# Kernel tuning notes

Measured on AMD Instinct MI355X. Metric: run time of the kernel, lower is better.

The kernel has to match this reference:

```python
import jax, jax.numpy as jnp
import numpy as np

NUM_HEADS = 16
HEAD_DIM = 128  # 2048 / 16


def setup_inputs() -> dict:
    key = jax.random.key(0)
    ks = jax.random.split(key, 5)
    B, S, D = 2, 2048, 2048
    scale = 1.0 / np.sqrt(D)
    return {
        "x": jax.random.normal(ks[0], (B, S, D), dtype=jnp.float32),
        "Wq": jax.random.normal(ks[1], (D, D), dtype=jnp.float32) * scale,
        "Wk": jax.random.normal(ks[2], (D, D), dtype=jnp.float32) * scale,
        "Wv": jax.random.normal(ks[3], (D, D), dtype=jnp.float32) * scale,
        "Wo": jax.random.normal(ks[4], (D, D), dtype=jnp.float32) * scale,
    }


def reference(x, Wq, Wk, Wv, Wo):
    B, S, D = x.shape
    H, Hd = NUM_HEADS, HEAD_DIM
    # nn.Linear(bias=False): y = x @ W.T
    q = (x @ Wq.T).reshape(B, S, H, Hd).transpose(0, 2, 1, 3)  # [B,H,S,Hd]
    k = (x @ Wk.T).reshape(B, S, H, Hd).transpose(0, 2, 1, 3)
    v = (x @ Wv.T).reshape(B, S, H, Hd).transpose(0, 2, 1, 3)
    scores = jnp.einsum("bhqd,bhkd->bhqk", q, k) / jnp.sqrt(jnp.float32(Hd))
    attn = jax.nn.softmax(scores, axis=-1)  # dropout p=0 (eval) -> identity
    out = jnp.einsum("bhqk,bhkd->bhqd", attn, v)  # [B,H,S,Hd]
    out = out.transpose(0, 2, 1, 3).reshape(B, S, D)
    out = out @ Wo.T
    return out
```

## Files before the change

kernel.cpp:

```cpp
#include <hip/hip_runtime.h>
#include <math.h>
#include <stdint.h>


#define DDIM 2048
#define SEQ  2048
#define NH   16
#define HD   128

typedef __attribute__((ext_vector_type(4))) float f32x4;
typedef __attribute__((ext_vector_type(16))) float f32x16;
typedef __attribute__((ext_vector_type(8))) __bf16 bf16x8;
typedef __attribute__((ext_vector_type(4))) unsigned int u32x4;
typedef __attribute__((ext_vector_type(2))) unsigned int u32x2;

#define MFMA_B16(a, b, c) __builtin_amdgcn_mfma_f32_16x16x32_bf16((a), (b), (c), 0, 0, 0)
#define MFMA32(a, b, c) __builtin_amdgcn_mfma_f32_32x32x16_bf16((a), (b), (c), 0, 0, 0)

__device__ __forceinline__ void async16(const void* g, void* l) {
  __builtin_amdgcn_global_load_lds(
      (const __attribute__((address_space(1))) unsigned int*)g,
      (__attribute__((address_space(3))) unsigned int*)l, 16, 0, 0);
}

__device__ __forceinline__ unsigned short f2bf(float f) {
  unsigned u = __builtin_bit_cast(unsigned, f);
  u += 0x7fffu + ((u >> 16) & 1u);
  return (unsigned short)(u >> 16);
}

__device__ __forceinline__ bf16x8 ldfrag(const unsigned short* p) {
  return __builtin_bit_cast(bf16x8, *(const u32x4*)p);
}

__device__ __forceinline__ void cvt_body(const float* __restrict__ s,
                                         unsigned short* __restrict__ d, int i) {
  const f32x4* sp = (const f32x4*)s;
  f32x4 a = sp[2 * i], b = sp[2 * i + 1];
  u32x4 o;
  o.x = ((unsigned)f2bf(a.y) << 16) | f2bf(a.x);
  o.y = ((unsigned)f2bf(a.w) << 16) | f2bf(a.z);
  o.z = ((unsigned)f2bf(b.y) << 16) | f2bf(b.x);
  o.w = ((unsigned)f2bf(b.w) << 16) | f2bf(b.z);
  ((u32x4*)d)[i] = o;
}

__global__ __launch_bounds__(256) void cvt_bf16_kernel(const float* __restrict__ s,
                                                       unsigned short* __restrict__ d) {
  cvt_body(s, d, blockIdx.x * 256 + threadIdx.x);
}

__global__ __launch_bounds__(256) void cvt_all_kernel(const float* __restrict__ x,
                                                      const float* __restrict__ wq,
                                                      const float* __restrict__ wk,
                                                      const float* __restrict__ wv,
                                                      const float* __restrict__ wo,
                                                      unsigned short* __restrict__ xb,
                                                      unsigned short* __restrict__ wqkv,
                                                      unsigned short* __restrict__ wob) {
  const int b = blockIdx.x;
  if (b < 4096) {
    cvt_body(x, xb, b * 256 + threadIdx.x);
  } else if (b < 10240) {
    const int wi = (b - 4096) >> 11, lb = (b - 4096) & 2047;
    const float* s = (wi == 0) ? wq : (wi == 1) ? wk : wv;
    cvt_body(s, wqkv + (size_t)wi * 4194304u, lb * 256 + threadIdx.x);
  } else {
    cvt_body(wo, wob, (b - 10240) * 256 + threadIdx.x);
  }
}

#define STGA(BUF, KH, COL)                            \
  {                                                   \
    const int c_ = (COL) & 2047;                      \
    async16(pA[0] + c_, &As[BUF][KH][tid * 8]);       \
    async16(pA[1] + c_, &As[BUF][KH][4096 + tid * 8]);\
  }
#define STGB(BUF, KH, COL)                            \
  {                                                   \
    const int c_ = (COL) & 2047;                      \
    async16(pB[0] + c_, &Bs[BUF][KH][tid * 8]);       \
    async16(pB[1] + c_, &Bs[BUF][KH][4096 + tid * 8]);\
  }
#define VM8 asm volatile("s_waitcnt vmcnt(8)" ::: "memory")
#define VMNONE (void)0

#define PHASE(BUF, KH, NH, STAGE_STMT, WAIT_STMT)                 \
  {                                                               \
    if ((NH) == 0) {                                              \
      const unsigned short* pl = &As[BUF][KH][0];                 \
      _Pragma("unroll") for (int mf = 0; mf < 4; ++mf) {          \
        const int r = awbase + mf * 32;                           \
        af[mf][0] = ldfrag(pl + r * 32 + c0);                     \
        af[mf][1] = ldfrag(pl + r * 32 + c1);                     \
      }                                                           \
    }                                                             \
    {                                                             \
      const unsigned short* pl = &Bs[BUF][KH][0];                 \
      const int r = bwbase + (NH) * 32;                           \
      bf0 = ldfrag(pl + r * 32 + c0);                             \
      bf1 = ldfrag(pl + r * 32 + c1);                             \
    }                                                             \
    STAGE_STMT;                                                   \
    __builtin_amdgcn_s_barrier();                                 \
    asm volatile("s_waitcnt lgkmcnt(0)" ::: "memory");            \
    __builtin_amdgcn_sched_barrier(0);                            \
    __builtin_amdgcn_s_setprio(1);                                \
    _Pragma("unroll") for (int mf = 0; mf < 4; ++mf) {            \
      acc[mf][NH] = MFMA32(af[mf][0], bf0, acc[mf][NH]);          \
      acc[mf][NH] = MFMA32(af[mf][1], bf1, acc[mf][NH]);          \
    }                                                             \
    __builtin_amdgcn_s_setprio(0);                                \
    WAIT_STMT;                                                    \
    __builtin_amdgcn_s_barrier();                                 \
  }

__global__ __launch_bounds__(512) void gemm_qkv8(const unsigned short* __restrict__ A,
                                                 const unsigned short* __restrict__ B,
                                                 unsigned short* __restrict__ Oqk,
                                                 unsigned short* __restrict__ Ovt,
                                                 float alpha_q) {
  __shared__ unsigned short As[2][2][256 * 32];
  __shared__ unsigned short Bs[2][2][256 * 32];
  const int tid = threadIdx.x;
  const int lane = tid & 63, w = tid >> 6;
  const int l32 = lane & 31, half = lane >> 5;
  const int wr = w >> 2, wc = w & 3;
  const int bm = blockIdx.y * 256, bn = blockIdx.x * 256;

  const int f2 = (l32 >> 1) & 3;
  const int c0 = (half ^ f2) * 8;
  const int c1 = ((2 + half) ^ f2) * 8;
  const int awbase = wr * 128 + l32;
  const int bwbase = wc * 64 + l32;

  f32x16 acc[4][2];
#pragma unroll
  for (int mf = 0; mf < 4; ++mf)
#pragma unroll
    for (int nf = 0; nf < 2; ++nf)
#pragma unroll
      for (int e = 0; e < 16; ++e) acc[mf][nf][e] = 0.f;

  bf16x8 af[4][2];
  bf16x8 bf0, bf1;

  const unsigned short* pA[2];
  const unsigned short* pB[2];
#pragma unroll
  for (int j = 0; j < 2; ++j) {
    const int slot = j * 512 + tid;
    const int row = slot >> 2, cs = slot & 3;
    const int g = cs ^ ((row >> 1) & 3);
    pA[j] = A + (size_t)(bm + row) * DDIM + g * 8;
    pB[j] = B + (size_t)(bn + row) * DDIM + g * 8;
  }

  STGA(0, 0, 0);
  STGB(0, 0, 0);
  STGA(0, 1, 32);
  STGB(0, 1, 32);
  STGA(1, 0, 64);
  STGB(1, 0, 64);
  asm volatile("s_waitcnt vmcnt(8)" ::: "memory");
  __builtin_amdgcn_s_barrier();

#pragma unroll 1
  for (int j = 0; j < 16; ++j) {
    const int cb = j * 128;
    PHASE(0, 0, 0, STGA(1, 1, cb + 96), VMNONE);
    PHASE(0, 0, 1, STGB(1, 1, cb + 96), VM8);
    PHASE(0, 1, 0, STGA(0, 0, cb + 128), VMNONE);
    PHASE(0, 1, 1, STGB(0, 0, cb + 128), VM8);
    PHASE(1, 0, 0, STGA(0, 1, cb + 160), VMNONE);
    PHASE(1, 0, 1, STGB(0, 1, cb + 160), VM8);
    PHASE(1, 1, 0, STGA(1, 0, cb + 192), VMNONE);
    PHASE(1, 1, 1, STGB(1, 0, cb + 192), VM8);
  }
  asm volatile("s_waitcnt vmcnt(0)" ::: "memory");

  const int seg = bn >> 11;
  const int bnl = bn & 2047;
  const float alpha = (seg == 0) ? alpha_q : 1.0f;
#pragma unroll
  for (int mf = 0; mf < 4; ++mf) {
#pragma unroll
    for (int nf = 0; nf < 2; ++nf) {
#pragma unroll
      for (int rg = 0; rg < 4; ++rg) {
        const int m0 = bm + wr * 128 + mf * 32 + rg * 8 + half * 4;
        const float v0 = acc[mf][nf][rg * 4 + 0] * alpha;
        const float v1 = acc[mf][nf][rg * 4 + 1] * alpha;
        const float v2 = acc[mf][nf][rg * 4 + 2] * alpha;
        const float v3 = acc[mf][nf][rg * 4 + 3] * alpha;
        const int n = bnl + wc * 64 + nf * 32 + l32;
        if (seg < 2) {
          unsigned short* O = Oqk + (size_t)seg * (4096u * 2048u);
          O[(size_t)(m0 + 0) * DDIM + n] = f2bf(v0);
          O[(size_t)(m0 + 1) * DDIM + n] = f2bf(v1);
          O[(size_t)(m0 + 2) * DDIM + n] = f2bf(v2);
          O[(size_t)(m0 + 3) * DDIM + n] = f2bf(v3);
        } else {
          const int bb = m0 >> 11, s0 = m0 & 2047;
          const int hh = n >> 7, dd = n & 127;
          u32x2 st;
          st.x = ((unsigned)f2bf(v1) << 16) | f2bf(v0);
          st.y = ((unsigned)f2bf(v3) << 16) | f2bf(v2);
          *(u32x2*)&Ovt[((size_t)((bb * NH + hh) * HD + dd)) * SEQ + s0] = st;
        }
      }
    }
  }
}

__global__ __launch_bounds__(256) void gemm_o64(const unsigned short* __restrict__ A,
                                                const unsigned short* __restrict__ B,
                                                float* __restrict__ Cf) {
  __shared__ unsigned short As[128 * 64];
  __shared__ unsigned short Bs[64 * 64];
  const int tid = threadIdx.x;
  const int lane = tid & 63, w = tid >> 6;
  const int l32 = lane & 31, half = lane >> 5;
  const int wm = (w >> 1) * 64, wn = (w & 1) * 32;
  const int bm = blockIdx.y * 128, bn = blockIdx.x * 64;

  f32x16 acc[2];
#pragma unroll
  for (int i = 0; i < 2; ++i)
#pragma unroll
    for (int e = 0; e < 16; ++e) acc[i][e] = 0.f;

  const unsigned short* pa[4];
  const unsigned short* pbb[2];
  {
#pragma unroll
    for (int j = 0; j < 4; ++j) {
      const int row = j * 32 + (tid >> 3);
      const int cg = (tid & 7) ^ (row & 7) ^ ((row >> 3) & 7);
      pa[j] = A + (size_t)(bm + row) * DDIM + cg * 8;
      if (j < 2) pbb[j] = B + (size_t)(bn + row) * DDIM + cg * 8;
    }
  }

  const int fr = (l32 & 7) ^ (l32 >> 3);
  const int fb = fr ^ ((wn >> 3) & 4);

  for (int kt = 0; kt < 32; ++kt) {
    __syncthreads();
#pragma unroll
    for (int j = 0; j < 4; ++j) {
      async16(pa[j], &As[(j * 256 + tid) * 8]);
      pa[j] += 64;
      if (j < 2) {
        async16(pbb[j], &Bs[(j * 256 + tid) * 8]);
        pbb[j] += 64;
      }
    }
    __syncthreads();
#pragma unroll
    for (int ks = 0; ks < 4; ++ks) {
      const int ph = ks * 2 + half;
      bf16x8 af0 = ldfrag(&As[(wm + l32) * 64 + (ph ^ fr) * 8]);
      bf16x8 af1 = ldfrag(&As[(wm + 32 + l32) * 64 + (ph ^ fr ^ 4) * 8]);
      bf16x8 bf0 = ldfrag(&Bs[(wn + l32) * 64 + (ph ^ fb) * 8]);
      acc[0] = MFMA32(af0, bf0, acc[0]);
      acc[1] = MFMA32(af1, bf0, acc[1]);
    }
  }

#pragma unroll
  for (int i = 0; i < 2; ++i) {
#pragma unroll
    for (int rg = 0; rg < 4; ++rg) {
      const int m0 = bm + wm + i * 32 + rg * 8 + half * 4;
      const int n = bn + wn + l32;
      Cf[(size_t)(m0 + 0) * DDIM + n] = acc[i][rg * 4 + 0];
      Cf[(size_t)(m0 + 1) * DDIM + n] = acc[i][rg * 4 + 1];
      Cf[(size_t)(m0 + 2) * DDIM + n] = acc[i][rg * 4 + 2];
      Cf[(size_t)(m0 + 3) * DDIM + n] = acc[i][rg * 4 + 3];
    }
  }
}

__global__ __launch_bounds__(512) void attn_kernel(const unsigned short* __restrict__ qb,
                                                   const unsigned short* __restrict__ kb,
                                                   const unsigned short* __restrict__ vtb,
                                                   unsigned short* __restrict__ ab) {
  __shared__ unsigned short Ks[64 * 128];
  __shared__ unsigned short Vts[128 * 64];
  __shared__ unsigned short Pw[8 * 16 * 40];
  const int tid = threadIdx.x;
  const int w = tid >> 6, lane = tid & 63;
  const int quad = lane >> 4, l16 = lane & 15;
  const int qt = blockIdx.x, bh = blockIdx.y;
  const int b = bh >> 4, h = bh & 15;
  const int qrow = qt * 128 + w * 16 + l16;

  const unsigned short* qp = qb + ((size_t)(b * SEQ + qrow)) * DDIM + h * HD;
  bf16x8 qf[4];
#pragma unroll
  for (int ks = 0; ks < 4; ++ks) qf[ks] = ldfrag(qp + ks * 32 + quad * 8);

  f32x4 ot[8];
#pragma unroll
  for (int i = 0; i < 8; i++) ot[i] = f32x4{0.f, 0.f, 0.f, 0.f};
  float sumacc = 0.f;

  const unsigned short* kp[2];
  const unsigned short* vp[2];
  {
    const size_t kbase = ((size_t)(b * SEQ)) * DDIM + h * HD;
    const size_t vbase = ((size_t)((b * NH + h) * HD)) * SEQ;
#pragma unroll
    for (int j = 0; j < 2; ++j) {
      const int key = j * 32 + (tid >> 4), cgk = (tid & 15) ^ (key & 15);
      kp[j] = kb + kbase + (size_t)key * DDIM + cgk * 8;
      const int dd = j * 64 + (tid >> 3), cgv = (tid & 7) ^ (dd & 7);
      vp[j] = vtb + vbase + (size_t)dd * SEQ + cgv * 8;
    }
  }
  unsigned short* pw = &Pw[w * 640];

  for (int kt = 0; kt < SEQ / 64; ++kt) {
    __syncthreads();
#pragma unroll
    for (int j = 0; j < 2; ++j) {
      async16(kp[j], &Ks[(j * 512 + tid) * 8]);
      kp[j] += (size_t)64 * DDIM;
      async16(vp[j], &Vts[(j * 512 + tid) * 8]);
      vp[j] += 64;
    }
    __syncthreads();
    f32x4 s[4];
#pragma unroll
    for (int t = 0; t < 4; ++t) s[t] = f32x4{0.f, 0.f, 0.f, 0.f};
#pragma unroll
    for (int ks = 0; ks < 4; ++ks) {
      const int sl = ((ks * 4 + quad) ^ l16) * 8;
#pragma unroll
      for (int t = 0; t < 4; ++t) {
        bf16x8 a = ldfrag(&Ks[(t * 16 + l16) * 128 + sl]);
        s[t] = MFMA_B16(a, qf[ks], s[t]);
      }
    }
    f32x4 p[4];
#pragma unroll
    for (int t = 0; t < 4; ++t) {
      p[t].x = __builtin_amdgcn_exp2f(s[t].x);
      p[t].y = __builtin_amdgcn_exp2f(s[t].y);
      p[t].z = __builtin_amdgcn_exp2f(s[t].z);
      p[t].w = __builtin_amdgcn_exp2f(s[t].w);
      sumacc += (p[t].x + p[t].y) + (p[t].z + p[t].w);
    }
    bf16x8 pb0, pb1;
    {
      u32x2 w0, w1;
      w0.x = ((unsigned)f2bf(p[0].y) << 16) | f2bf(p[0].x);
      w0.y = ((unsigned)f2bf(p[0].w) << 16) | f2bf(p[0].z);
      w1.x = ((unsigned)f2bf(p[1].y) << 16) | f2bf(p[1].x);
      w1.y = ((unsigned)f2bf(p[1].w) << 16) | f2bf(p[1].z);
      *(u32x2*)&pw[l16 * 40 + quad * 4] = w0;
      *(u32x2*)&pw[l16 * 40 + 16 + quad * 4] = w1;
      asm volatile("s_waitcnt lgkmcnt(0)" ::: "memory");
      pb0 = ldfrag(&pw[l16 * 40 + quad * 8]);
      w0.x = ((unsigned)f2bf(p[2].y) << 16) | f2bf(p[2].x);
      w0.y = ((unsigned)f2bf(p[2].w) << 16) | f2bf(p[2].z);
      w1.x = ((unsigned)f2bf(p[3].y) << 16) | f2bf(p[3].x);
      w1.y = ((unsigned)f2bf(p[3].w) << 16) | f2bf(p[3].z);
      *(u32x2*)&pw[l16 * 40 + quad * 4] = w0;
      *(u32x2*)&pw[l16 * 40 + 16 + quad * 4] = w1;
      asm volatile("s_waitcnt lgkmcnt(0)" ::: "memory");
      pb1 = ldfrag(&pw[l16 * 40 + quad * 8]);
    }
#pragma unroll
    for (int mt = 0; mt < 8; ++mt) {
      bf16x8 vf0 = ldfrag(&Vts[(mt * 16 + l16) * 64 + (quad ^ (l16 & 7)) * 8]);
      ot[mt] = MFMA_B16(vf0, pb0, ot[mt]);
      bf16x8 vf1 = ldfrag(&Vts[(mt * 16 + l16) * 64 + ((4 + quad) ^ (l16 & 7)) * 8]);
      ot[mt] = MFMA_B16(vf1, pb1, ot[mt]);
    }
  }
  float total = sumacc;
  total += __shfl_xor(total, 16);
  total += __shfl_xor(total, 32);
  const float inv = 1.0f / total;
  unsigned short* op = ab + ((size_t)(b * SEQ + qrow)) * DDIM + h * HD;
#pragma unroll
  for (int mt = 0; mt < 8; ++mt) {
    f32x4 v = ot[mt] * inv;
    u32x2 st;
    st.x = ((unsigned)f2bf(v.y) << 16) | f2bf(v.x);
    st.y = ((unsigned)f2bf(v.w) << 16) | f2bf(v.z);
    *(u32x2*)&op[mt * 16 + quad * 4] = st;
  }
}

extern "C" void kernel_launch(void* const* d_in, const int* in_sizes, int n_in,
                              void* d_out, int out_size, void* d_ws, size_t ws_size,
                              hipStream_t stream) {
  (void)in_sizes; (void)n_in; (void)out_size;
  const float* x = (const float*)d_in[0];
  const float* Wq = (const float*)d_in[1];
  const float* Wk = (const float*)d_in[2];
  const float* Wv = (const float*)d_in[3];
  const float* Wo = (const float*)d_in[4];

  char* ws = (char*)d_ws;
  unsigned short* xb = (unsigned short*)(ws);
  unsigned short* wqkv = (unsigned short*)(ws + 16777216);
  unsigned short* qb = (unsigned short*)(ws + 41943040);
  unsigned short* kb = (unsigned short*)(ws + 58720256);
  unsigned short* vtb = (unsigned short*)(ws + 75497472);
  const bool big = ws_size >= 100663296ull;
  unsigned short* wob = big ? (unsigned short*)(ws + 92274688) : wqkv;

  const float alpha_q = 1.44269504088896341f / sqrtf(128.0f);

  if (big) {
    cvt_all_kernel<<<dim3(12288), 256, 0, stream>>>(x, Wq, Wk, Wv, Wo, xb, wqkv, wob);
    gemm_qkv8<<<dim3(24, 16), 512, 0, stream>>>(xb, wqkv, qb, vtb, alpha_q);
  } else {
    cvt_all_kernel<<<dim3(10240), 256, 0, stream>>>(x, Wq, Wk, Wv, Wo, xb, wqkv, wob);
    gemm_qkv8<<<dim3(24, 16), 512, 0, stream>>>(xb, wqkv, qb, vtb, alpha_q);
    cvt_bf16_kernel<<<dim3(2048), 256, 0, stream>>>(Wo, wob);
  }

  attn_kernel<<<dim3(16, 32), 512, 0, stream>>>(qb, kb, vtb, xb);

  gemm_o64<<<dim3(32, 32), 256, 0, stream>>>(xb, wob, (float*)d_out);
}
```

Baseline: 411.4 us.

## Restructure QKV GEMM into double-buffered K=64 tiles with new LDS swizzle

Replaces the four-slot K=32 half-tile staging pipeline in the QKV projection GEMM with a two-buffer K=64 tile scheme. Each tile is consumed in four MFMA phases while the next tile is prefetched asynchronously into the other buffer. A new 8-way XOR swizzle is used for LDS rows and fragment reads. The aim is simpler indexing and fewer, larger transfers, but waiting with vmcnt(0) once per tile shortens how far ahead loads run, which may expose global-load latency.

```diff
diff --git a/kernel.cpp b/kernel.cpp
--- a/kernel.cpp
+++ b/kernel.cpp
@@ -70,49 +70,43 @@
   }
 }
 
-#define STGA(BUF, KH, COL)                            \
-  {                                                   \
-    const int c_ = (COL) & 2047;                      \
-    async16(pA[0] + c_, &As[BUF][KH][tid * 8]);       \
-    async16(pA[1] + c_, &As[BUF][KH][4096 + tid * 8]);\
-  }
-#define STGB(BUF, KH, COL)                            \
-  {                                                   \
-    const int c_ = (COL) & 2047;                      \
-    async16(pB[0] + c_, &Bs[BUF][KH][tid * 8]);       \
-    async16(pB[1] + c_, &Bs[BUF][KH][4096 + tid * 8]);\
-  }
-#define VM8 asm volatile("s_waitcnt vmcnt(8)" ::: "memory")
+#define STG_A(NXT, HOFF, CB)                                              \
+  {                                                                       \
+    async16(pA[0] + (HOFF) * DDIM + (CB), &As[NXT][(HOFF) * 64 + tid * 8]); \
+    async16(pA[1] + (HOFF) * DDIM + (CB),                                 \
+            &As[NXT][(HOFF) * 64 + 4096 + tid * 8]);                      \
+  }
+#define STG_B(NXT, HOFF, CB)                                              \
+  {                                                                       \
+    async16(pB[0] + (HOFF) * DDIM + (CB), &Bs[NXT][(HOFF) * 64 + tid * 8]); \
+    async16(pB[1] + (HOFF) * DDIM + (CB),                                 \
+            &Bs[NXT][(HOFF) * 64 + 4096 + tid * 8]);                      \
+  }
+#define VM0 asm volatile("s_waitcnt vmcnt(0)" ::: "memory")
 #define VMNONE (void)0
 
-#define PHASE(BUF, KH, NH, STAGE_STMT, WAIT_STMT)                 \
-  {                                                               \
-    if ((NH) == 0) {                                              \
-      const unsigned short* pl = &As[BUF][KH][0];                 \
-      _Pragma("unroll") for (int mf = 0; mf < 4; ++mf) {          \
-        const int r = awbase + mf * 32;                           \
-        af[mf][0] = ldfrag(pl + r * 32 + c0);                     \
-        af[mf][1] = ldfrag(pl + r * 32 + c1);                     \
-      }                                                           \
-    }                                                             \
-    {                                                             \
-      const unsigned short* pl = &Bs[BUF][KH][0];                 \
-      const int r = bwbase + (NH) * 32;                           \
-      bf0 = ldfrag(pl + r * 32 + c0);                             \
-      bf1 = ldfrag(pl + r * 32 + c1);                             \
-    }                                                             \
-    STAGE_STMT;                                                   \
-    __builtin_amdgcn_s_barrier();                                 \
-    asm volatile("s_waitcnt lgkmcnt(0)" ::: "memory");            \
-    __builtin_amdgcn_sched_barrier(0);                            \
-    __builtin_amdgcn_s_setprio(1);                                \
-    _Pragma("unroll") for (int mf = 0; mf < 4; ++mf) {            \
-      acc[mf][NH] = MFMA32(af[mf][0], bf0, acc[mf][NH]);          \
-      acc[mf][NH] = MFMA32(af[mf][1], bf1, acc[mf][NH]);          \
-    }                                                             \
-    __builtin_amdgcn_s_setprio(0);                                \
-    WAIT_STMT;                                                    \
-    __builtin_amdgcn_s_barrier();                                 \
+#define PHASE2(CUR, KS, STAGE_STMT, WAIT_STMT)                        \
+  {                                                                   \
+    const int ph = (KS) * 2 + half;                                   \
+    bf16x8 af_[4], bf_[2];                                            \
+    _Pragma("unroll") for (int mf = 0; mf < 4; ++mf) af_[mf] =        \
+        ldfrag(&As[CUR][(wr * 128 + mf * 32 + l32) * 64 +             \
+                        (ph ^ fr ^ ((mf & 1) * 4)) * 8]);             \
+    _Pragma("unroll") for (int nf = 0; nf < 2; ++nf) bf_[nf] =        \
+        ldfrag(&Bs[CUR][(wc * 64 + nf * 32 + l32) * 64 +              \
+                        (ph ^ fr ^ (nf * 4)) * 8]);                   \
+    STAGE_STMT;                                                       \
+    __builtin_amdgcn_s_barrier();                                     \
+    asm volatile("s_waitcnt lgkmcnt(0)" ::: "memory");                \
+    __builtin_amdgcn_sched_barrier(0);                                \
+    __builtin_amdgcn_s_setprio(1);                                    \
+    _Pragma("unroll") for (int mf = 0; mf < 4; ++mf) {                \
+      acc[mf][0] = MFMA32(af_[mf], bf_[0], acc[mf][0]);               \
+      acc[mf][1] = MFMA32(af_[mf], bf_[1], acc[mf][1]);               \
+    }                                                                 \
+    __builtin_amdgcn_s_setprio(0);                                    \
+    WAIT_STMT;                                                        \
+    __builtin_amdgcn_s_barrier();                                     \
   }
 
 __global__ __launch_bounds__(512) void gemm_qkv8(const unsigned short* __restrict__ A,
@@ -120,19 +114,15 @@
                                                  unsigned short* __restrict__ Oqk,
                                                  unsigned short* __restrict__ Ovt,
                                                  float alpha_q) {
-  __shared__ unsigned short As[2][2][256 * 32];
-  __shared__ unsigned short Bs[2][2][256 * 32];
+  __shared__ unsigned short As[2][256 * 64];
+  __shared__ unsigned short Bs[2][256 * 64];
   const int tid = threadIdx.x;
   const int lane = tid & 63, w = tid >> 6;
   const int l32 = lane & 31, half = lane >> 5;
   const int wr = w >> 2, wc = w & 3;
   const int bm = blockIdx.y * 256, bn = blockIdx.x * 256;
 
-  const int f2 = (l32 >> 1) & 3;
-  const int c0 = (half ^ f2) * 8;
-  const int c1 = ((2 + half) ^ f2) * 8;
-  const int awbase = wr * 128 + l32;
-  const int bwbase = wc * 64 + l32;
+  const int fr = (l32 & 7) ^ (l32 >> 3);
 
   f32x16 acc[4][2];
 #pragma unroll
@@ -141,43 +131,34 @@
     for (int nf = 0; nf < 2; ++nf)
 #pragma unroll
       for (int e = 0; e < 16; ++e) acc[mf][nf][e] = 0.f;
-
-  bf16x8 af[4][2];
-  bf16x8 bf0, bf1;
 
   const unsigned short* pA[2];
   const unsigned short* pB[2];
 #pragma unroll
   for (int j = 0; j < 2; ++j) {
     const int slot = j * 512 + tid;
-    const int row = slot >> 2, cs = slot & 3;
-    const int g = cs ^ ((row >> 1) & 3);
-    pA[j] = A + (size_t)(bm + row) * DDIM + g * 8;
-    pB[j] = B + (size_t)(bn + row) * DDIM + g * 8;
-  }
-
-  STGA(0, 0, 0);
-  STGB(0, 0, 0);
-  STGA(0, 1, 32);
-  STGB(0, 1, 32);
-  STGA(1, 0, 64);
-  STGB(1, 0, 64);
-  asm volatile("s_waitcnt vmcnt(8)" ::: "memory");
+    const int rowl = slot >> 3, cs = slot & 7;
+    const int g = cs ^ (rowl & 7) ^ ((rowl >> 3) & 7);
+    pA[j] = A + (size_t)(bm + rowl) * DDIM + g * 8;
+    pB[j] = B + (size_t)(bn + rowl) * DDIM + g * 8;
+  }
+
+  STG_A(0, 0, 0);
+  STG_A(0, 128, 0);
+  STG_B(0, 0, 0);
+  STG_B(0, 128, 0);
+  asm volatile("s_waitcnt vmcnt(0)" ::: "memory");
   __builtin_amdgcn_s_barrier();
 
 #pragma unroll 1
-  for (int j = 0; j < 16; ++j) {
-    const int cb = j * 128;
-    PHASE(0, 0, 0, STGA(1, 1, cb + 96), VMNONE);
-    PHASE(0, 0, 1, STGB(1, 1, cb + 96), VM8);
-    PHASE(0, 1, 0, STGA(0, 0, cb + 128), VMNONE);
-    PHASE(0, 1, 1, STGB(0, 0, cb + 128), VM8);
-    PHASE(1, 0, 0, STGA(0, 1, cb + 160), VMNONE);
-    PHASE(1, 0, 1, STGB(0, 1, cb + 160), VM8);
-    PHASE(1, 1, 0, STGA(1, 0, cb + 192), VMNONE);
-    PHASE(1, 1, 1, STGB(1, 0, cb + 192), VM8);
-  }
-  asm volatile("s_waitcnt vmcnt(0)" ::: "memory");
+  for (int kt = 0; kt < 32; ++kt) {
+    const int cur = kt & 1, nxt = cur ^ 1;
+    const int cb = ((kt + 1) & 31) * 64;
+    PHASE2(cur, 0, { STG_A(nxt, 0, cb); STG_A(nxt, 128, cb); }, VMNONE);
+    PHASE2(cur, 1, { STG_B(nxt, 0, cb); STG_B(nxt, 128, cb); }, VMNONE);
+    PHASE2(cur, 2, VMNONE, VMNONE);
+    PHASE2(cur, 3, VMNONE, VM0);
+  }
 
   const int seg = bn >> 11;
   const int bnl = bn & 2047;
```

Result: faster. 391.6 us (-4.8%).
